# Kernel optimization log

Hardware: AMD Instinct MI355X
Metric: run time of the kernel (lower is better)

Reference implementation:

```python
import jax, jax.numpy as jnp
import numpy as np
from jax import lax

B, T, F, D, K = 64, 1000, 140, 256, 7
TAU, V_TH, EPS, ALPHA = 2.0, 1.0, 1e-5, 2.0
PAD = (K - 1) // 2

# Heaviside spike with ATan surrogate gradient (spikingjelly default, alpha=2)
@jax.custom_vjp
def spike_fn(x):
    return (x >= 0.0).astype(x.dtype)

def _spike_fwd(x):
    return spike_fn(x), x

def _spike_bwd(x, g):
    sg = (ALPHA / 2.0) / (1.0 + (jnp.pi / 2.0 * ALPHA * x) ** 2)
    return (g * sg,)

spike_fn.defvjp(_spike_fwd, _spike_bwd)

def lif(x_seq):
    """Multi-step LIF: v += (x - v)/tau, hard reset to 0 on spike. x_seq: (T,B,D)."""
    def step(v, x):
        v = v + (x - v) / TAU
        s = spike_fn(v - V_TH)
        return v * (1.0 - s), s
    _, spikes = lax.scan(step, jnp.zeros_like(x_seq[0]), x_seq)
    return spikes

def bn(x, g, b, m, v):
    # eval-mode BatchNorm1d over channel dim D (last axis of (T,B,D))
    return (x - m) * (g * lax.rsqrt(v + EPS)) + b

def setup_inputs() -> dict:
    key = jax.random.key(0)
    ks = jax.random.split(key, 4)
    s = 0.05
    return {
        "x": jax.random.normal(ks[0], (B, T, F), jnp.float32),
        "pw_w": jax.random.normal(ks[1], (D, F), jnp.float32) * s,
        "pw_b": jnp.zeros((D,), jnp.float32),
        "dw_w": jax.random.normal(ks[2], (D, 1, K), jnp.float32) * s,  # depthwise (O,I/g,K)
        "bn1_g": jnp.ones((D,), jnp.float32),
        "bn1_b": jnp.zeros((D,), jnp.float32),
        "bn1_m": jnp.zeros((D,), jnp.float32),
        "bn1_v": jnp.ones((D,), jnp.float32),
        "lin_w": jax.random.normal(ks[3], (D, D), jnp.float32) * s,
        "bn2_g": jnp.ones((D,), jnp.float32),
        "bn2_b": jnp.zeros((D,), jnp.float32),
        "bn2_m": jnp.zeros((D,), jnp.float32),
        "bn2_v": jnp.ones((D,), jnp.float32),
    }

def reference(x, pw_w, pw_b, dw_w, bn1_g, bn1_b, bn1_m, bn1_v,
              lin_w, bn2_g, bn2_b, bn2_m, bn2_v):
    # pointwise conv: (B,T,F) -> (B,D,T)
    h = jnp.einsum('btf,df->bdt', x, pw_w) + pw_b[None, :, None]
    # depthwise temporal conv, groups=D, same padding
    h = lax.conv_general_dilated(h, dw_w, window_strides=(1,),
                                 padding=[(PAD, PAD)], feature_group_count=D,
                                 dimension_numbers=('NCH', 'OIH', 'NCH'))
    h = jnp.transpose(h, (2, 0, 1))  # (T,B,D) multi-step layout
    h = lif(bn(h, bn1_g, bn1_b, bn1_m, bn1_v))
    residual = h
    h = jnp.einsum('tbd,ed->tbe', h, lin_w)
    h = lif(bn(h, bn2_g, bn2_b, bn2_m, bn2_v))
    return h + residual
```

## Files before the change

### kernel.cpp

```cpp
#include <hip/hip_runtime.h>
#include <hip/hip_bf16.h>

#define B_  64
#define T_  1000
#define F_  140
#define D_  256
#define EPS_ 1e-5f

#define CL_ 50
#define NC_ 20
#define W_  24

#define CW_  95
#define NCH_ 11

typedef __attribute__((ext_vector_type(8))) short bf16x8;
typedef __attribute__((ext_vector_type(4))) short bf16x4;
typedef __attribute__((ext_vector_type(4))) float f32x4;

static __device__ inline short f2bf(float f) {
  __hip_bfloat16 h = __float2bfloat16(f);
  return *reinterpret_cast<short*>(&h);
}
static __device__ inline float bf2f(short s) {
  unsigned int u = ((unsigned int)(unsigned short)s) << 16;
  return __uint_as_float(u);
}

__global__ __launch_bounds__(256) void k0_prep(const float* __restrict__ lw,
                                               float* __restrict__ lwT,
                                               const float* __restrict__ pw,
                                               short* __restrict__ wbf) {
  int i = blockIdx.x * 256 + threadIdx.x;
  if (i < 65536) {
    int e = i >> 8, d = i & 255;
    lwT[(size_t)d * D_ + e] = lw[(size_t)e * D_ + d];
  } else if (i < 65536 + 256 * 160) {
    int j = i - 65536;
    int n = j / 160, k = j - n * 160;
    wbf[j] = (k < F_) ? f2bf(pw[(size_t)n * F_ + k]) : (short)0;
  }
}

__global__ __launch_bounds__(256, 2) void k12_fused(const float* __restrict__ x,
                                                    const short* __restrict__ wbf,
                                                    const float* __restrict__ bias,
                                                    const float* __restrict__ dww,
                                                    const float* __restrict__ g1,
                                                    const float* __restrict__ b1,
                                                    const float* __restrict__ m1,
                                                    const float* __restrict__ v1,
                                                    unsigned long long* __restrict__ bits) {
  __shared__ short smem[32768];
  short* As = smem;
  short* Bs = smem + 10240;
  const int b = blockIdx.x;
  const int c = blockIdx.y;
  const int a = CW_ * c;
  const int tid = threadIdx.x;
  const int lane = tid & 63, wv = tid >> 6;
  const int lr = lane & 15, quad = lane >> 4;
  const int mr = (wv & 1) * 64;
  const int nc0 = (wv >> 1) * 128;

  const int srow = tid >> 1;
  const int sc4 = (tid & 1) * 4;
  const bool arow_ok = (a + srow) < T_;
  const float* xrow = x + ((size_t)b * T_ + a + srow) * F_;
  const short* wsrc0 = wbf + (size_t)tid * 160;

  auto stage = [&](int kc, int buf) {
    short* abase = As + buf * (128 * 40) + srow * 40;
#pragma unroll
    for (int s = 0; s < 4; s++) {
      int c4 = sc4 + s;
      int kg = kc + c4 * 4;
      float4 av = make_float4(0.f, 0.f, 0.f, 0.f);
      if (arow_ok && kg < F_) av = *(const float4*)(xrow + kg);
      bf16x4 pk = {f2bf(av.x), f2bf(av.y), f2bf(av.z), f2bf(av.w)};
      *(bf16x4*)(abase + c4 * 4) = pk;
    }
    short* bbase = Bs + buf * (256 * 40) + tid * 40;
    const short* wsrc = wsrc0 + kc;
#pragma unroll
    for (int s = 0; s < 4; s++)
      *(bf16x8*)(bbase + s * 8) = *(const bf16x8*)(wsrc + s * 8);
  };

  f32x4 acc[4][8] = {};
  stage(0, 0);
  __syncthreads();
#pragma unroll
  for (int kk = 0; kk < 5; kk++) {
    const int cur = kk & 1;
    if (kk < 4) stage((kk + 1) * 32, cur ^ 1);
    const short* ap = As + cur * (128 * 40) + quad * 8;
    const short* bp = Bs + cur * (256 * 40) + quad * 8;
    bf16x8 af[4], bfr[8];
#pragma unroll
    for (int i = 0; i < 4; i++) af[i] = *(const bf16x8*)(ap + (mr + i * 16 + lr) * 40);
#pragma unroll
    for (int j = 0; j < 8; j++) bfr[j] = *(const bf16x8*)(bp + (nc0 + j * 16 + lr) * 40);
#pragma unroll
    for (int i = 0; i < 4; i++)
#pragma unroll
      for (int j = 0; j < 8; j++)
        acc[i][j] = __builtin_amdgcn_mfma_f32_16x16x32_bf16(af[i], bfr[j], acc[i][j], 0, 0, 0);
    __syncthreads();
  }

  short* hbuf = smem;
  if (c == 0) {
    hbuf[0 * D_ + tid] = 0; hbuf[1 * D_ + tid] = 0; hbuf[2 * D_ + tid] = 0;
  }
#pragma unroll
  for (int j = 0; j < 8; j++) {
    const int n = nc0 + j * 16 + lr;
    const float badd = bias[n];
#pragma unroll
    for (int i = 0; i < 4; i++) {
      const int m = mr + i * 16 + quad * 4;
#pragma unroll
      for (int r = 0; r < 4; r++) {
        const int mm = m + r;
        if (mm < 125) {
          short val = ((a + mm) < T_) ? f2bf(acc[i][j][r] + badd) : (short)0;
          hbuf[(mm + 3) * D_ + n] = val;
        }
      }
    }
  }
  __syncthreads();

  const int d = tid;
  float w[7];
#pragma unroll
  for (int k = 0; k < 7; k++) w[k] = dww[d * 7 + k];
  const float sc = g1[d] * rsqrtf(v1[d] + EPS_);
  const float shf = b1[d] - m1[d] * sc;

  const int lt0 = (c == 0) ? 0 : 3;
  const int nwarm = (c == 0) ? 0 : W_;
  const int tw0 = a + ((c == 0) ? 0 : 27);
  int nwrite = (c == 0) ? 122 : CW_;
  if (nwrite > T_ - tw0) nwrite = T_ - tw0;

  float win0 = bf2f(hbuf[(lt0 + 0) * D_ + d]);
  float win1 = bf2f(hbuf[(lt0 + 1) * D_ + d]);
  float win2 = bf2f(hbuf[(lt0 + 2) * D_ + d]);
  float win3 = bf2f(hbuf[(lt0 + 3) * D_ + d]);
  float win4 = bf2f(hbuf[(lt0 + 4) * D_ + d]);
  float win5 = bf2f(hbuf[(lt0 + 5) * D_ + d]);
  float v = 0.f;
  int s = 0;
  for (; s < nwarm; s++) {
    float tap6 = bf2f(hbuf[(lt0 + s + 6) * D_ + d]);
    float conv = win0 * w[0] + win1 * w[1] + win2 * w[2] + win3 * w[3] +
                 win4 * w[4] + win5 * w[5] + tap6 * w[6];
    float u = conv * sc + shf;
    v = 0.5f * (v + u);
    v = (v >= 1.0f) ? 0.f : v;
    win0 = win1; win1 = win2; win2 = win3; win3 = win4; win4 = win5; win5 = tap6;
  }
  unsigned long long* bp2 = bits + ((size_t)b * T_ + tw0) * 4 + wv;
  const bool lane0 = (lane == 0);
  for (int i2 = 0; i2 < nwrite; i2++, s++) {
    float tap6 = bf2f(hbuf[(lt0 + s + 6) * D_ + d]);
    float conv = win0 * w[0] + win1 * w[1] + win2 * w[2] + win3 * w[3] +
                 win4 * w[4] + win5 * w[5] + tap6 * w[6];
    float u = conv * sc + shf;
    v = 0.5f * (v + u);
    bool sp = (v >= 1.0f);
    unsigned long long mask = __ballot(sp);
    if (lane0) bp2[(size_t)i2 * 4] = mask;
    v = sp ? 0.f : v;
    win0 = win1; win1 = win2; win2 = win3; win3 = win4; win4 = win5; win5 = tap6;
  }
}

__global__ __launch_bounds__(256) void k3_lin_lif(const unsigned long long* __restrict__ bits,
                                                  const float* __restrict__ lwT,
                                                  const float* __restrict__ g2,
                                                  const float* __restrict__ b2,
                                                  const float* __restrict__ m2,
                                                  const float* __restrict__ v2,
                                                  float* __restrict__ out) {
  __shared__ unsigned long long sb[(CL_ + W_) * 4];
  const int b = blockIdx.x;
  const int t0 = blockIdx.y * CL_;
  const int tstart = (t0 >= W_) ? t0 - W_ : 0;
  const int nwarm = t0 - tstart;
  const int nsteps = nwarm + CL_;
  const int e = threadIdx.x;
  const unsigned long long* gbp = bits + ((size_t)b * T_ + tstart) * 4;
  for (int i = e; i < nsteps * 4; i += 256) sb[i] = gbp[i];
  __syncthreads();

  const float sc = g2[e] * rsqrtf(v2[e] + EPS_);
  const float shf = b2[e] - m2[e] * sc;
  const int eq = e >> 6, eb = e & 63;
  float v = 0.f;
  int s = 0;
  for (; s < nwarm; s++) {
    unsigned long long w0 = sb[s * 4 + 0], w1 = sb[s * 4 + 1];
    unsigned long long w2 = sb[s * 4 + 2], w3 = sb[s * 4 + 3];
    float acc = 0.f;
    if (w0 | w1 | w2 | w3) {
      unsigned long long mm;
      mm = w0; while (mm) { int l = __builtin_ctzll(mm); mm &= mm - 1; acc += lwT[(size_t)(l) * D_ + e]; }
      mm = w1; while (mm) { int l = __builtin_ctzll(mm); mm &= mm - 1; acc += lwT[(size_t)(64 + l) * D_ + e]; }
      mm = w2; while (mm) { int l = __builtin_ctzll(mm); mm &= mm - 1; acc += lwT[(size_t)(128 + l) * D_ + e]; }
      mm = w3; while (mm) { int l = __builtin_ctzll(mm); mm &= mm - 1; acc += lwT[(size_t)(192 + l) * D_ + e]; }
    }
    float u = acc * sc + shf;
    v = 0.5f * (v + u);
    v = (v >= 1.0f) ? 0.f : v;
  }
  float* op = out + ((size_t)t0 * B_ + b) * D_ + e;
  const size_t ts = (size_t)B_ * D_;
#pragma unroll 5
  for (int i = 0; i < CL_; i++, s++) {
    unsigned long long w0 = sb[s * 4 + 0], w1 = sb[s * 4 + 1];
    unsigned long long w2 = sb[s * 4 + 2], w3 = sb[s * 4 + 3];
    float acc = 0.f;
    if (w0 | w1 | w2 | w3) {
      unsigned long long mm;
      mm = w0; while (mm) { int l = __builtin_ctzll(mm); mm &= mm - 1; acc += lwT[(size_t)(l) * D_ + e]; }
      mm = w1; while (mm) { int l = __builtin_ctzll(mm); mm &= mm - 1; acc += lwT[(size_t)(64 + l) * D_ + e]; }
      mm = w2; while (mm) { int l = __builtin_ctzll(mm); mm &= mm - 1; acc += lwT[(size_t)(128 + l) * D_ + e]; }
      mm = w3; while (mm) { int l = __builtin_ctzll(mm); mm &= mm - 1; acc += lwT[(size_t)(192 + l) * D_ + e]; }
    }
    float u = acc * sc + shf;
    v = 0.5f * (v + u);
    bool sp = (v >= 1.0f);
    unsigned long long myw = sb[s * 4 + eq];
    float s1 = (float)((myw >> eb) & 1ull);
    op[(size_t)i * ts] = (sp ? 1.0f : 0.0f) + s1;
    v = sp ? 0.f : v;
  }
}

extern "C" void kernel_launch(void* const* d_in, const int* in_sizes, int n_in,
                              void* d_out, int out_size, void* d_ws, size_t ws_size,
                              hipStream_t stream) {
  const float* x    = (const float*)d_in[0];
  const float* pw_w = (const float*)d_in[1];
  const float* pw_b = (const float*)d_in[2];
  const float* dw_w = (const float*)d_in[3];
  const float* g1   = (const float*)d_in[4];
  const float* b1   = (const float*)d_in[5];
  const float* m1   = (const float*)d_in[6];
  const float* v1   = (const float*)d_in[7];
  const float* lw   = (const float*)d_in[8];
  const float* g2   = (const float*)d_in[9];
  const float* b2   = (const float*)d_in[10];
  const float* m2   = (const float*)d_in[11];
  const float* v2   = (const float*)d_in[12];
  float* out = (float*)d_out;

  char* ws = (char*)d_ws;
  unsigned long long* bits = (unsigned long long*)ws;
  float* lwT = (float*)(ws + 2048000);
  short* wbf = (short*)(ws + 2048000 + 262144);

  k0_prep<<<(65536 + 256 * 160 + 255) / 256, 256, 0, stream>>>(lw, lwT, pw_w, wbf);
  dim3 g_k12(B_, NCH_);
  k12_fused<<<g_k12, 256, 0, stream>>>(x, wbf, pw_b, dw_w, g1, b1, m1, v1, bits);
  dim3 g_k3(B_, NC_);
  k3_lin_lif<<<g_k3, 256, 0, stream>>>(bits, lwT, g2, b2, m2, v2, out);
}
```

Measured before the change: 169.2 us.

## Split fused conv kernel across channel halves and batch LIF loads

The fused pointwise-GEMM/depthwise/LIF kernel now splits the 256 channels into two halves via a third grid dimension. Each block computes a 128x128 tile with a smaller shared buffer, giving twice as many blocks and higher occupancy. The time-chunk geometry is changed to 96-step chunks with a fixed 27-row history. BN scale and the 0.5 LIF factor are folded into the conv weights, and the recurrent loops are unrolled with batched shared-memory loads. In the second kernel, bit words are prefetched in groups and reused for the residual. Only half the threads run the sequential LIF phase in k12, so per-block serial work stays the same while overlapping GEMM work across channel halves is duplicated for the A operand.

```diff
diff --git a/kernel.cpp b/kernel.cpp
--- a/kernel.cpp
+++ b/kernel.cpp
@@ -11,12 +11,13 @@
 #define NC_ 20
 #define W_  24
 
-#define CW_  95
+#define CW2_ 96
 #define NCH_ 11
+#define HST_ 132
 
 typedef __attribute__((ext_vector_type(8))) short bf16x8;
-typedef __attribute__((ext_vector_type(4))) short bf16x4;
 typedef __attribute__((ext_vector_type(4))) float f32x4;
+typedef unsigned long long u64;
 
 static __device__ inline short f2bf(float f) {
   __hip_bfloat16 h = __float2bfloat16(f);
@@ -42,157 +43,166 @@
   }
 }
 
-__global__ __launch_bounds__(256, 2) void k12_fused(const float* __restrict__ x,
-                                                    const short* __restrict__ wbf,
-                                                    const float* __restrict__ bias,
-                                                    const float* __restrict__ dww,
-                                                    const float* __restrict__ g1,
-                                                    const float* __restrict__ b1,
-                                                    const float* __restrict__ m1,
-                                                    const float* __restrict__ v1,
-                                                    unsigned long long* __restrict__ bits) {
-  __shared__ short smem[32768];
+__global__ __launch_bounds__(256) void k12_fused(const float* __restrict__ x,
+                                                 const short* __restrict__ wbf,
+                                                 const float* __restrict__ bias,
+                                                 const float* __restrict__ dww,
+                                                 const float* __restrict__ g1,
+                                                 const float* __restrict__ b1,
+                                                 const float* __restrict__ m1,
+                                                 const float* __restrict__ v1,
+                                                 u64* __restrict__ bits) {
+  __shared__ short smem[20480];
   short* As = smem;
   short* Bs = smem + 10240;
   const int b = blockIdx.x;
   const int c = blockIdx.y;
-  const int a = CW_ * c;
+  const int half = blockIdx.z;
+  const int n0g = half * 128;
+  const int tb = CW2_ * c - 27;
   const int tid = threadIdx.x;
   const int lane = tid & 63, wv = tid >> 6;
   const int lr = lane & 15, quad = lane >> 4;
-  const int mr = (wv & 1) * 64;
-  const int nc0 = (wv >> 1) * 128;
+  const int mr = (wv & 1) * 64, nc0 = (wv >> 1) * 64;
 
   const int srow = tid >> 1;
-  const int sc4 = (tid & 1) * 4;
-  const bool arow_ok = (a + srow) < T_;
-  const float* xrow = x + ((size_t)b * T_ + a + srow) * F_;
-  const short* wsrc0 = wbf + (size_t)tid * 160;
+  const int kh = (tid & 1) * 16;
+  const int ta = tb + srow;
+  const bool arow_ok = (ta >= 0) && (ta < T_);
+  const float* xrow = x + ((size_t)b * T_ + ta) * F_;
+  const short* wrow = wbf + (size_t)(n0g + srow) * 160 + kh;
 
   auto stage = [&](int kc, int buf) {
-    short* abase = As + buf * (128 * 40) + srow * 40;
-#pragma unroll
-    for (int s = 0; s < 4; s++) {
-      int c4 = sc4 + s;
-      int kg = kc + c4 * 4;
+    short tmp[16];
+#pragma unroll
+    for (int q = 0; q < 4; q++) {
+      int kg = kc + kh + q * 4;
       float4 av = make_float4(0.f, 0.f, 0.f, 0.f);
       if (arow_ok && kg < F_) av = *(const float4*)(xrow + kg);
-      bf16x4 pk = {f2bf(av.x), f2bf(av.y), f2bf(av.z), f2bf(av.w)};
-      *(bf16x4*)(abase + c4 * 4) = pk;
-    }
-    short* bbase = Bs + buf * (256 * 40) + tid * 40;
-    const short* wsrc = wsrc0 + kc;
-#pragma unroll
-    for (int s = 0; s < 4; s++)
-      *(bf16x8*)(bbase + s * 8) = *(const bf16x8*)(wsrc + s * 8);
+      tmp[q * 4 + 0] = f2bf(av.x); tmp[q * 4 + 1] = f2bf(av.y);
+      tmp[q * 4 + 2] = f2bf(av.z); tmp[q * 4 + 3] = f2bf(av.w);
+    }
+    short* ap = As + buf * 5120 + srow * 40 + kh;
+    *(bf16x8*)(ap + 0) = *(bf16x8*)(tmp + 0);
+    *(bf16x8*)(ap + 8) = *(bf16x8*)(tmp + 8);
+    short* bp = Bs + buf * 5120 + srow * 40 + kh;
+    *(bf16x8*)(bp + 0) = *(const bf16x8*)(wrow + kc + 0);
+    *(bf16x8*)(bp + 8) = *(const bf16x8*)(wrow + kc + 8);
   };
 
-  f32x4 acc[4][8] = {};
+  f32x4 acc[4][4] = {};
   stage(0, 0);
   __syncthreads();
 #pragma unroll
   for (int kk = 0; kk < 5; kk++) {
     const int cur = kk & 1;
     if (kk < 4) stage((kk + 1) * 32, cur ^ 1);
-    const short* ap = As + cur * (128 * 40) + quad * 8;
-    const short* bp = Bs + cur * (256 * 40) + quad * 8;
-    bf16x8 af[4], bfr[8];
+    const short* ap = As + cur * 5120 + quad * 8;
+    const short* bp = Bs + cur * 5120 + quad * 8;
+    bf16x8 af[4], bfr[4];
 #pragma unroll
     for (int i = 0; i < 4; i++) af[i] = *(const bf16x8*)(ap + (mr + i * 16 + lr) * 40);
 #pragma unroll
-    for (int j = 0; j < 8; j++) bfr[j] = *(const bf16x8*)(bp + (nc0 + j * 16 + lr) * 40);
+    for (int j = 0; j < 4; j++) bfr[j] = *(const bf16x8*)(bp + (nc0 + j * 16 + lr) * 40);
 #pragma unroll
     for (int i = 0; i < 4; i++)
 #pragma unroll
-      for (int j = 0; j < 8; j++)
+      for (int j = 0; j < 4; j++)
         acc[i][j] = __builtin_amdgcn_mfma_f32_16x16x32_bf16(af[i], bfr[j], acc[i][j], 0, 0, 0);
     __syncthreads();
   }
 
   short* hbuf = smem;
-  if (c == 0) {
-    hbuf[0 * D_ + tid] = 0; hbuf[1 * D_ + tid] = 0; hbuf[2 * D_ + tid] = 0;
-  }
-#pragma unroll
-  for (int j = 0; j < 8; j++) {
+#pragma unroll
+  for (int j = 0; j < 4; j++) {
     const int n = nc0 + j * 16 + lr;
-    const float badd = bias[n];
+    const float badd = bias[n0g + n];
 #pragma unroll
     for (int i = 0; i < 4; i++) {
       const int m = mr + i * 16 + quad * 4;
 #pragma unroll
       for (int r = 0; r < 4; r++) {
-        const int mm = m + r;
-        if (mm < 125) {
-          short val = ((a + mm) < T_) ? f2bf(acc[i][j][r] + badd) : (short)0;
-          hbuf[(mm + 3) * D_ + n] = val;
+        const int t = tb + m + r;
+        short val = (t >= 0 && t < T_) ? f2bf(acc[i][j][r] + badd) : (short)0;
+        hbuf[(m + r) * HST_ + n] = val;
+      }
+    }
+  }
+  __syncthreads();
+
+  if (tid < 128) {
+    const int d = n0g + tid;
+    const float scv = g1[d] * rsqrtf(v1[d] + EPS_);
+    float w2[7];
+#pragma unroll
+    for (int k = 0; k < 7; k++) w2[k] = dww[d * 7 + k] * (0.5f * scv);
+    const float sh2 = 0.5f * (b1[d] - m1[d] * scv);
+
+    const int wb = (c == 0) ? 24 : 0;
+    float win0 = bf2f(hbuf[(wb + 0) * HST_ + tid]);
+    float win1 = bf2f(hbuf[(wb + 1) * HST_ + tid]);
+    float win2 = bf2f(hbuf[(wb + 2) * HST_ + tid]);
+    float win3 = bf2f(hbuf[(wb + 3) * HST_ + tid]);
+    float win4 = bf2f(hbuf[(wb + 4) * HST_ + tid]);
+    float win5 = bf2f(hbuf[(wb + 5) * HST_ + tid]);
+    float v = 0.f;
+
+    if (c != 0) {
+#pragma unroll
+      for (int s0 = 0; s0 < 24; s0 += 8) {
+        float tap[8];
+#pragma unroll
+        for (int g = 0; g < 8; g++) tap[g] = bf2f(hbuf[(s0 + g + 6) * HST_ + tid]);
+#pragma unroll
+        for (int g = 0; g < 8; g++) {
+          float u2 = win0 * w2[0] + win1 * w2[1] + win2 * w2[2] + win3 * w2[3] +
+                     win4 * w2[4] + win5 * w2[5] + tap[g] * w2[6] + sh2;
+          v = 0.5f * v + u2;
+          v = (v >= 1.0f) ? 0.f : v;
+          win0 = win1; win1 = win2; win2 = win3; win3 = win4; win4 = win5; win5 = tap[g];
         }
       }
     }
-  }
-  __syncthreads();
-
-  const int d = tid;
-  float w[7];
-#pragma unroll
-  for (int k = 0; k < 7; k++) w[k] = dww[d * 7 + k];
-  const float sc = g1[d] * rsqrtf(v1[d] + EPS_);
-  const float shf = b1[d] - m1[d] * sc;
-
-  const int lt0 = (c == 0) ? 0 : 3;
-  const int nwarm = (c == 0) ? 0 : W_;
-  const int tw0 = a + ((c == 0) ? 0 : 27);
-  int nwrite = (c == 0) ? 122 : CW_;
-  if (nwrite > T_ - tw0) nwrite = T_ - tw0;
-
-  float win0 = bf2f(hbuf[(lt0 + 0) * D_ + d]);
-  float win1 = bf2f(hbuf[(lt0 + 1) * D_ + d]);
-  float win2 = bf2f(hbuf[(lt0 + 2) * D_ + d]);
-  float win3 = bf2f(hbuf[(lt0 + 3) * D_ + d]);
-  float win4 = bf2f(hbuf[(lt0 + 4) * D_ + d]);
-  float win5 = bf2f(hbuf[(lt0 + 5) * D_ + d]);
-  float v = 0.f;
-  int s = 0;
-  for (; s < nwarm; s++) {
-    float tap6 = bf2f(hbuf[(lt0 + s + 6) * D_ + d]);
-    float conv = win0 * w[0] + win1 * w[1] + win2 * w[2] + win3 * w[3] +
-                 win4 * w[4] + win5 * w[5] + tap6 * w[6];
-    float u = conv * sc + shf;
-    v = 0.5f * (v + u);
-    v = (v >= 1.0f) ? 0.f : v;
-    win0 = win1; win1 = win2; win2 = win3; win3 = win4; win4 = win5; win5 = tap6;
-  }
-  unsigned long long* bp2 = bits + ((size_t)b * T_ + tw0) * 4 + wv;
-  const bool lane0 = (lane == 0);
-  for (int i2 = 0; i2 < nwrite; i2++, s++) {
-    float tap6 = bf2f(hbuf[(lt0 + s + 6) * D_ + d]);
-    float conv = win0 * w[0] + win1 * w[1] + win2 * w[2] + win3 * w[3] +
-                 win4 * w[4] + win5 * w[5] + tap6 * w[6];
-    float u = conv * sc + shf;
-    v = 0.5f * (v + u);
-    bool sp = (v >= 1.0f);
-    unsigned long long mask = __ballot(sp);
-    if (lane0) bp2[(size_t)i2 * 4] = mask;
-    v = sp ? 0.f : v;
-    win0 = win1; win1 = win2; win2 = win3; win3 = win4; win4 = win5; win5 = tap6;
-  }
-}
-
-__global__ __launch_bounds__(256) void k3_lin_lif(const unsigned long long* __restrict__ bits,
+    const int tw0 = CW2_ * c;
+    const int dq = half * 2 + (tid >> 6);
+    u64* bp2 = bits + ((size_t)b * T_ + tw0) * 4 + dq;
+    const bool lane0 = ((tid & 63) == 0);
+    const int smax = T_ - tw0;
+#pragma unroll
+    for (int s0 = 0; s0 < 96; s0 += 8) {
+      float tap[8];
+#pragma unroll
+      for (int g = 0; g < 8; g++) tap[g] = bf2f(hbuf[(s0 + g + 30) * HST_ + tid]);
+#pragma unroll
+      for (int g = 0; g < 8; g++) {
+        float u2 = win0 * w2[0] + win1 * w2[1] + win2 * w2[2] + win3 * w2[3] +
+                   win4 * w2[4] + win5 * w2[5] + tap[g] * w2[6] + sh2;
+        v = 0.5f * v + u2;
+        bool sp = (v >= 1.0f);
+        u64 mask = __ballot(sp);
+        if (lane0 && (s0 + g) < smax) bp2[(size_t)(s0 + g) * 4] = mask;
+        v = sp ? 0.f : v;
+        win0 = win1; win1 = win2; win2 = win3; win3 = win4; win4 = win5; win5 = tap[g];
+      }
+    }
+  }
+}
+
+__global__ __launch_bounds__(256) void k3_lin_lif(const u64* __restrict__ bits,
                                                   const float* __restrict__ lwT,
                                                   const float* __restrict__ g2,
                                                   const float* __restrict__ b2,
                                                   const float* __restrict__ m2,
                                                   const float* __restrict__ v2,
                                                   float* __restrict__ out) {
-  __shared__ unsigned long long sb[(CL_ + W_) * 4];
+  __shared__ u64 sb[(CL_ + W_) * 4];
   const int b = blockIdx.x;
   const int t0 = blockIdx.y * CL_;
   const int tstart = (t0 >= W_) ? t0 - W_ : 0;
   const int nwarm = t0 - tstart;
   const int nsteps = nwarm + CL_;
   const int e = threadIdx.x;
-  const unsigned long long* gbp = bits + ((size_t)b * T_ + tstart) * 4;
+  const u64* gbp = bits + ((size_t)b * T_ + tstart) * 4;
   for (int i = e; i < nsteps * 4; i += 256) sb[i] = gbp[i];
   __syncthreads();
 
@@ -200,43 +210,63 @@
   const float shf = b2[e] - m2[e] * sc;
   const int eq = e >> 6, eb = e & 63;
   float v = 0.f;
-  int s = 0;
-  for (; s < nwarm; s++) {
-    unsigned long long w0 = sb[s * 4 + 0], w1 = sb[s * 4 + 1];
-    unsigned long long w2 = sb[s * 4 + 2], w3 = sb[s * 4 + 3];
-    float acc = 0.f;
-    if (w0 | w1 | w2 | w3) {
-      unsigned long long mm;
-      mm = w0; while (mm) { int l = __builtin_ctzll(mm); mm &= mm - 1; acc += lwT[(size_t)(l) * D_ + e]; }
-      mm = w1; while (mm) { int l = __builtin_ctzll(mm); mm &= mm - 1; acc += lwT[(size_t)(64 + l) * D_ + e]; }
-      mm = w2; while (mm) { int l = __builtin_ctzll(mm); mm &= mm - 1; acc += lwT[(size_t)(128 + l) * D_ + e]; }
-      mm = w3; while (mm) { int l = __builtin_ctzll(mm); mm &= mm - 1; acc += lwT[(size_t)(192 + l) * D_ + e]; }
-    }
-    float u = acc * sc + shf;
-    v = 0.5f * (v + u);
-    v = (v >= 1.0f) ? 0.f : v;
+
+  if (nwarm) {
+#pragma unroll
+    for (int s0 = 0; s0 < 24; s0 += 4) {
+      u64 a0[4], a1[4], a2[4], a3[4];
+#pragma unroll
+      for (int g = 0; g < 4; g++) {
+        a0[g] = sb[(s0 + g) * 4 + 0]; a1[g] = sb[(s0 + g) * 4 + 1];
+        a2[g] = sb[(s0 + g) * 4 + 2]; a3[g] = sb[(s0 + g) * 4 + 3];
+      }
+#pragma unroll
+      for (int g = 0; g < 4; g++) {
+        float u = shf;
+        if (a0[g] | a1[g] | a2[g] | a3[g]) {
+          float acc = 0.f;
+          u64 mm;
+          mm = a0[g]; while (mm) { int l = __builtin_ctzll(mm); mm &= mm - 1; acc += lwT[(size_t)(l) * D_ + e]; }
+          mm = a1[g]; while (mm) { int l = __builtin_ctzll(mm); mm &= mm - 1; acc += lwT[(size_t)(64 + l) * D_ + e]; }
+          mm = a2[g]; while (mm) { int l = __builtin_ctzll(mm); mm &= mm - 1; acc += lwT[(size_t)(128 + l) * D_ + e]; }
+          mm = a3[g]; while (mm) { int l = __builtin_ctzll(mm); mm &= mm - 1; acc += lwT[(size_t)(192 + l) * D_ + e]; }
+          u = acc * sc + shf;
+        }
+        v = 0.5f * (v + u);
+        v = (v >= 1.0f) ? 0.f : v;
+      }
+    }
   }
   float* op = out + ((size_t)t0 * B_ + b) * D_ + e;
   const size_t ts = (size_t)B_ * D_;
-#pragma unroll 5
-  for (int i = 0; i < CL_; i++, s++) {
-    unsigned long long w0 = sb[s * 4 + 0], w1 = sb[s * 4 + 1];
-    unsigned long long w2 = sb[s * 4 + 2], w3 = sb[s * 4 + 3];
-    float acc = 0.f;
-    if (w0 | w1 | w2 | w3) {
-      unsigned long long mm;
-      mm = w0; while (mm) { int l = __builtin_ctzll(mm); mm &= mm - 1; acc += lwT[(size_t)(l) * D_ + e]; }
-      mm = w1; while (mm) { int l = __builtin_ctzll(mm); mm &= mm - 1; acc += lwT[(size_t)(64 + l) * D_ + e]; }
-      mm = w2; while (mm) { int l = __builtin_ctzll(mm); mm &= mm - 1; acc += lwT[(size_t)(128 + l) * D_ + e]; }
-      mm = w3; while (mm) { int l = __builtin_ctzll(mm); mm &= mm - 1; acc += lwT[(size_t)(192 + l) * D_ + e]; }
-    }
-    float u = acc * sc + shf;
-    v = 0.5f * (v + u);
-    bool sp = (v >= 1.0f);
-    unsigned long long myw = sb[s * 4 + eq];
-    float s1 = (float)((myw >> eb) & 1ull);
-    op[(size_t)i * ts] = (sp ? 1.0f : 0.0f) + s1;
-    v = sp ? 0.f : v;
+#pragma unroll
+  for (int s0 = 0; s0 < 50; s0 += 5) {
+    u64 a0[5], a1[5], a2[5], a3[5];
+#pragma unroll
+    for (int g = 0; g < 5; g++) {
+      const int s = nwarm + s0 + g;
+      a0[g] = sb[s * 4 + 0]; a1[g] = sb[s * 4 + 1];
+      a2[g] = sb[s * 4 + 2]; a3[g] = sb[s * 4 + 3];
+    }
+#pragma unroll
+    for (int g = 0; g < 5; g++) {
+      float u = shf;
+      if (a0[g] | a1[g] | a2[g] | a3[g]) {
+        float acc = 0.f;
+        u64 mm;
+        mm = a0[g]; while (mm) { int l = __builtin_ctzll(mm); mm &= mm - 1; acc += lwT[(size_t)(l) * D_ + e]; }
+        mm = a1[g]; while (mm) { int l = __builtin_ctzll(mm); mm &= mm - 1; acc += lwT[(size_t)(64 + l) * D_ + e]; }
+        mm = a2[g]; while (mm) { int l = __builtin_ctzll(mm); mm &= mm - 1; acc += lwT[(size_t)(128 + l) * D_ + e]; }
+        mm = a3[g]; while (mm) { int l = __builtin_ctzll(mm); mm &= mm - 1; acc += lwT[(size_t)(192 + l) * D_ + e]; }
+        u = acc * sc + shf;
+      }
+      v = 0.5f * (v + u);
+      bool sp = (v >= 1.0f);
+      u64 myw = (eq == 0) ? a0[g] : (eq == 1) ? a1[g] : (eq == 2) ? a2[g] : a3[g];
+      float s1 = (float)((myw >> eb) & 1ull);
+      op[(size_t)(s0 + g) * ts] = (sp ? 1.0f : 0.0f) + s1;
+      v = sp ? 0.f : v;
+    }
   }
 }
 
@@ -259,12 +289,12 @@
   float* out = (float*)d_out;
 
   char* ws = (char*)d_ws;
-  unsigned long long* bits = (unsigned long long*)ws;
+  u64* bits = (u64*)ws;
   float* lwT = (float*)(ws + 2048000);
   short* wbf = (short*)(ws + 2048000 + 262144);
 
   k0_prep<<<(65536 + 256 * 160 + 255) / 256, 256, 0, stream>>>(lw, lwT, pw_w, wbf);
-  dim3 g_k12(B_, NCH_);
+  dim3 g_k12(B_, NCH_, 2);
   k12_fused<<<g_k12, 256, 0, stream>>>(x, wbf, pw_b, dw_w, g1, b1, m1, v1, bits);
   dim3 g_k3(B_, NC_);
   k3_lin_lif<<<g_k3, 256, 0, stream>>>(bits, lwT, g2, b2, m2, v2, out);
```

Measured after the change: 176.9 us. 4.5% more time.
